# Optimization experiments

Measured on AMD Instinct MI355X. Metric: run time of the kernel, lower is better.

The kernel has to match this reference:

```python
import jax, jax.numpy as jnp
import numpy as np

EPS = 1e-12  # torch F.normalize default eps

def l2norm(x, axis):
    n = jnp.sqrt(jnp.sum(x * x, axis=axis, keepdims=True))
    return x / jnp.maximum(n, EPS)

def conv2d(x, w, b, pad):
    y = jax.lax.conv_general_dilated(x, w, (1, 1), [(pad, pad), (pad, pad)],
                                     dimension_numbers=('NCHW', 'OIHW', 'NCHW'))
    return y + b[None, :, None, None]

def setup_inputs() -> dict:
    key = jax.random.key(0)
    ks = jax.random.split(key, 12)
    N, C, H, W, K = 16, 256, 64, 64, 32
    s = 0.05
    return {
        'feature':   jax.random.normal(ks[0], (N, C, H, W), jnp.float32),
        'conv_up_w': jax.random.normal(ks[1], (K, C, 3, 3), jnp.float32) * s,
        'conv_up_b': jax.random.normal(ks[2], (K,), jnp.float32) * s,
        'centroids': jax.random.uniform(ks[3], (K, C), jnp.float32),
        'upfc_w':    jax.random.normal(ks[4], (C, K * C), jnp.float32) * s,
        'upfc_b':    jax.random.normal(ks[5], (C,), jnp.float32) * s,
        't1_w':      jax.random.normal(ks[6], (C, 2 * C, 1, 1), jnp.float32) * s,
        't1_b':      jax.random.normal(ks[7], (C,), jnp.float32) * s,
        't2_w':      jax.random.normal(ks[8], (C, C, 1, 1), jnp.float32) * s,
        't2_b':      jax.random.normal(ks[9], (C,), jnp.float32) * s,
    }

def reference(feature, conv_up_w, conv_up_b, centroids, upfc_w, upfc_b, t1_w, t1_b, t2_w, t2_b):
    N, C, H, W = feature.shape
    K = centroids.shape[0]
    # --- UP branch ---
    xn = l2norm(feature, axis=1)                       # (N,C,H,W)
    sa = jax.nn.softmax(conv2d(xn, conv_up_w, conv_up_b, 1), axis=1)  # (N,K,H,W)
    sa_flat = sa.reshape(N, K, H * W)                  # (N,K,L)
    x_flat = xn.reshape(N, C, H * W)                   # (N,C,L)
    # sum_l sa[n,k,l] * (x[n,c,l] - centroid[k,c])  ==  two matmuls, no (N,K,C,L) tensor
    up = jnp.einsum('nkl,ncl->nkc', sa_flat, x_flat) \
         - jnp.sum(sa_flat, axis=-1)[:, :, None] * centroids[None]   # (N,K,C)
    up = l2norm(up, axis=2).reshape(N, K * C)
    up = l2norm(up, axis=1)
    up = up @ upfc_w.T + upfc_b                        # (N,C)
    up_map = jnp.broadcast_to(up[:, :, None, None], (N, C, H, W))
    # --- transform ---
    nf = jnp.concatenate([feature, up_map], axis=1)    # (N,2C,H,W)
    h = jax.nn.relu(conv2d(nf, t1_w, t1_b, 0))
    return jax.nn.relu(conv2d(h, t2_w, t2_b, 0))
```

## Files before the change

### kernel.cpp

```cpp
#include <hip/hip_runtime.h>
#include <cstdint>

#define N_ 16
#define C_ 256
#define H_ 64
#define W_ 64
#define L_ 4096
#define K_ 32
#define CL_ (C_*L_)
#define KL_ (K_*L_)
#define KC_ (K_*C_)

typedef __attribute__((ext_vector_type(8))) short short8;
typedef __attribute__((ext_vector_type(4))) float f32x4;

__device__ __forceinline__ unsigned short f2bf(float x) {
    unsigned int u = __float_as_uint(x);
    u += 0x7fffu + ((u >> 16) & 1u);
    return (unsigned short)(u >> 16);
}
__device__ __forceinline__ unsigned int pack2(float a, float b) {
    return (unsigned int)f2bf(a) | ((unsigned int)f2bf(b) << 16);
}

__device__ __forceinline__ void glds16(const void* g, void* l) {
    __builtin_amdgcn_global_load_lds(
        (const __attribute__((address_space(1))) unsigned int*)g,
        (__attribute__((address_space(3))) unsigned int*)l, 16, 0, 0);
}

__global__ __launch_bounds__(256) void k_prep(
    const float* __restrict__ f, float* __restrict__ rinv,
    unsigned short* __restrict__ xnb)
{
    __shared__ float tile[256 * 34];
    __shared__ float ssred[8 * 33];
    __shared__ float rbuf[32];
    int bid = blockIdx.x;
    int n = bid >> 7;
    int l0 = (bid & 127) << 5;
    int tid = threadIdx.x;
    int l = tid & 31, cb = tid >> 5;
    const float* fp = f + (size_t)n * CL_ + l0 + l;
    float ss = 0.f;
#pragma unroll
    for (int i = 0; i < 32; ++i) {
        int c = (cb << 5) + i;
        float v = fp[(size_t)c * L_];
        tile[c * 34 + l] = v;
        ss = fmaf(v, v, ss);
    }
    ssred[cb * 33 + l] = ss;
    __syncthreads();
    if (tid < 32) {
        float s = 0.f;
#pragma unroll
        for (int j = 0; j < 8; ++j) s += ssred[j * 33 + tid];
        float ri = 1.0f / fmaxf(sqrtf(s), 1e-12f);
        rinv[n * L_ + l0 + tid] = ri;
        rbuf[tid] = ri;
    }
    __syncthreads();
    float ri = rbuf[l];
    unsigned short* op = xnb + ((size_t)n * L_ + l0 + l) * C_ + (cb << 5);
#pragma unroll
    for (int g = 0; g < 4; ++g) {
        unsigned int pk[4];
#pragma unroll
        for (int d = 0; d < 4; ++d) {
            int c = (cb << 5) + (g << 3) + (d << 1);
            pk[d] = pack2(tile[c * 34 + l] * ri, tile[(c + 1) * 34 + l] * ri);
        }
        *(uint4*)(op + (g << 3)) = make_uint4(pk[0], pk[1], pk[2], pk[3]);
    }
}

__global__ __launch_bounds__(256) void k_wpack(const float* __restrict__ w, unsigned short* __restrict__ wb) {
    int i = blockIdx.x * 256 + threadIdx.x;
    int j = i & 7;
    int k = (i >> 3) & 31;
    int q = (i >> 8) & 3;
    int ch = (i >> 10) & 7;
    int t = i >> 13;
    int c = (ch << 5) + (q << 3) + j;
    wb[i] = f2bf(w[k * 2304 + c * 9 + t]);
}

__global__ __launch_bounds__(256) void k_wpack2(const float* __restrict__ w, int stride,
                                                unsigned short* __restrict__ wb) {
    int i = blockIdx.x * 256 + threadIdx.x;
    int co = i >> 8, ci = i & 255;
    wb[i] = f2bf(w[(size_t)co * stride + ci]);
}

__global__ __launch_bounds__(128, 2) void k_conv(
    const unsigned short* __restrict__ xnb, const unsigned short* __restrict__ wb,
    const float* __restrict__ bias, const float* __restrict__ zpad,
    float* __restrict__ sa, float* __restrict__ ssum)
{
    __shared__ __align__(16) unsigned short lsB[2][408 * 8];
    __shared__ __align__(16) unsigned short lsW[2][1152 * 8];
    __shared__ float sred[2][32];
    int bid = blockIdx.x;
    int n = bid & 15, y = (bid >> 4) & 63, px_b = bid >> 10;
    int tid = threadIdx.x;
    int wv = tid >> 6, lane = tid & 63;
    int r = lane & 15, quad = lane >> 4;
    int pxw = (wv << 4) + r;
    int xbase = (px_b << 5) - 1;
    const unsigned short* xb = xnb + (size_t)n * CL_;
    const unsigned short* zp = (const unsigned short*)zpad;

    const unsigned short* bsrc[4];
    bool bact[4];
#pragma unroll
    for (int k = 0; k < 4; ++k) {
        int c = (wv << 6) + (k << 7) + lane;
        bool act = c < 408;
        int cc = act ? c : 0;
        int row = cc / 136;
        int rem = cc - row * 136;
        int q = rem / 34;
        int px = rem - q * 34;
        int yy = y + row - 1, xx = xbase + px;
        bool ok = act && ((unsigned)yy < 64u) && ((unsigned)xx < 64u);
        bsrc[k] = ok ? (xb + (((size_t)(yy << 6) + xx) << 8) + (q << 3)) : zp;
        bact[k] = act;
    }

    f32x4 acc0 = (f32x4){0.f, 0.f, 0.f, 0.f};
    f32x4 acc1 = (f32x4){0.f, 0.f, 0.f, 0.f};

    {
#pragma unroll
        for (int k = 0; k < 4; ++k)
            if (bact[k]) glds16(bsrc[k], lsB[0] + (((wv << 6) + (k << 7)) << 3));
#pragma unroll
        for (int k = 0; k < 9; ++k) {
            int idx = wv * 9 + k;
            int t = idx >> 1, h = idx & 1;
            glds16(wb + (t << 13) + (h << 9) + (lane << 3), lsW[0] + (idx << 9));
        }
    }

    for (int i = 0; i < 8; ++i) {
        asm volatile("s_waitcnt vmcnt(0)" ::: "memory");
        __syncthreads();
        if (i < 7) {
            int c1 = (i + 1) << 5;
            unsigned short* dB = lsB[(i + 1) & 1];
            unsigned short* dW = lsW[(i + 1) & 1];
#pragma unroll
            for (int k = 0; k < 4; ++k)
                if (bact[k]) glds16(bsrc[k] + c1, dB + (((wv << 6) + (k << 7)) << 3));
#pragma unroll
            for (int k = 0; k < 9; ++k) {
                int idx = wv * 9 + k;
                int t = idx >> 1, h = idx & 1;
                glds16(wb + (t << 13) + (h << 9) + ((i + 1) << 10) + (lane << 3),
                       dW + (idx << 9));
            }
        }
        const unsigned short* bufB = lsB[i & 1];
        const unsigned short* bufW = lsW[i & 1];
#pragma unroll
        for (int dy = 0; dy < 3; ++dy) {
#pragma unroll
            for (int dx = 0; dx < 3; ++dx) {
                int t = dy * 3 + dx;
                short8 B  = *(const short8*)(bufB + ((((dy << 2) + quad) * 34 + (pxw + dx)) << 3));
                short8 A0 = *(const short8*)(bufW + (((t << 7) + (quad << 5) + r) << 3));
                short8 A1 = *(const short8*)(bufW + (((t << 7) + (quad << 5) + 16 + r) << 3));
                acc0 = __builtin_amdgcn_mfma_f32_16x16x32_bf16(A0, B, acc0, 0, 0, 0);
                acc1 = __builtin_amdgcn_mfma_f32_16x16x32_bf16(A1, B, acc1, 0, 0, 0);
            }
        }
    }
    float4 b0 = *(const float4*)(bias + (quad << 2));
    float4 b1 = *(const float4*)(bias + 16 + (quad << 2));
    float v[8];
    v[0] = acc0[0] + b0.x; v[1] = acc0[1] + b0.y; v[2] = acc0[2] + b0.z; v[3] = acc0[3] + b0.w;
    v[4] = acc1[0] + b1.x; v[5] = acc1[1] + b1.y; v[6] = acc1[2] + b1.z; v[7] = acc1[3] + b1.w;
    float mx = v[0];
#pragma unroll
    for (int j = 1; j < 8; ++j) mx = fmaxf(mx, v[j]);
    mx = fmaxf(mx, __shfl_xor(mx, 16));
    mx = fmaxf(mx, __shfl_xor(mx, 32));
    float s = 0.f;
#pragma unroll
    for (int j = 0; j < 8; ++j) { v[j] = __expf(v[j] - mx); s += v[j]; }
    s += __shfl_xor(s, 16);
    s += __shfl_xor(s, 32);
    float rs = 1.0f / s;
    float sv8[8];
#pragma unroll
    for (int j = 0; j < 8; ++j) sv8[j] = v[j] * rs;
    int l = (y << 6) + (px_b << 5) + pxw;
    float* sp = sa + (size_t)n * KL_ + l;
#pragma unroll
    for (int j = 0; j < 4; ++j) {
        sp[(size_t)((quad << 2) + j) * L_] = sv8[j];
        sp[(size_t)(16 + (quad << 2) + j) * L_] = sv8[4 + j];
    }
#pragma unroll
    for (int j = 0; j < 8; ++j) {
        float a = sv8[j];
        a += __shfl_xor(a, 1); a += __shfl_xor(a, 2);
        a += __shfl_xor(a, 4); a += __shfl_xor(a, 8);
        sv8[j] = a;
    }
    if (r == 0) {
#pragma unroll
        for (int j = 0; j < 4; ++j) {
            sred[wv][(quad << 2) + j] = sv8[j];
            sred[wv][16 + (quad << 2) + j] = sv8[4 + j];
        }
    }
    __syncthreads();
    if (tid < 32) {
        float t = sred[0][tid] + sred[1][tid];
        atomicAdd(ssum + n * K_ + tid, t);
    }
}

__global__ __launch_bounds__(256) void k_einsum(
    const float* __restrict__ f, const float* __restrict__ rinv,
    const float* __restrict__ sa, float* __restrict__ up)
{
    __shared__ float xn_s[C_ * 33];
    __shared__ float sa_s[K_ * 32];
    int bid = blockIdx.x;
    int n = bid >> 5;
    int l0 = (bid & 31) << 7;
    int tid = threadIdx.x;
    int kq = tid >> 5, cq = tid & 31;
    float acc[4][8];
#pragma unroll
    for (int i = 0; i < 4; ++i)
#pragma unroll
        for (int j = 0; j < 8; ++j) acc[i][j] = 0.f;

    for (int ch = 0; ch < 4; ++ch) {
        int lc = l0 + (ch << 5);
        __syncthreads();
        {
            int crow = tid >> 3, lq = (tid & 7) << 2;
#pragma unroll
            for (int p = 0; p < 8; ++p) {
                int c = (p << 5) + crow;
                float4 f4 = *(const float4*)(f + (size_t)n * CL_ + (size_t)c * L_ + lc + lq);
                float4 r4 = *(const float4*)(rinv + n * L_ + lc + lq);
                float* d = xn_s + c * 33 + lq;
                d[0] = f4.x * r4.x; d[1] = f4.y * r4.y; d[2] = f4.z * r4.z; d[3] = f4.w * r4.w;
            }
        }
        {
            int k = tid >> 3, lq = (tid & 7) << 2;
            float4 a4 = *(const float4*)(sa + (size_t)n * KL_ + (size_t)k * L_ + lc + lq);
            *(float4*)(sa_s + (k << 5) + lq) = a4;
        }
        __syncthreads();
#pragma unroll 4
        for (int l = 0; l < 32; ++l) {
            float sv[4], xv[8];
#pragma unroll
            for (int i = 0; i < 4; ++i) sv[i] = sa_s[((kq << 2) + i) * 32 + l];
#pragma unroll
            for (int j = 0; j < 8; ++j) xv[j] = xn_s[(cq + (j << 5)) * 33 + l];
#pragma unroll
            for (int i = 0; i < 4; ++i)
#pragma unroll
                for (int j = 0; j < 8; ++j) acc[i][j] = fmaf(sv[i], xv[j], acc[i][j]);
        }
    }
    float* upp = up + (size_t)n * KC_;
#pragma unroll
    for (int i = 0; i < 4; ++i)
#pragma unroll
        for (int j = 0; j < 8; ++j)
            atomicAdd(upp + ((kq << 2) + i) * C_ + cq + (j << 5), acc[i][j]);
}

__global__ __launch_bounds__(256) void k_rowfix(
    const float* __restrict__ up, const float* __restrict__ ssum,
    const float* __restrict__ cent, float* __restrict__ upn, float* __restrict__ rowss)
{
    __shared__ float red[256];
    int bid = blockIdx.x;
    int k = bid & 31;
    float sv = ssum[bid];
    float v = up[(size_t)bid * C_ + threadIdx.x] - sv * cent[k * C_ + threadIdx.x];
    red[threadIdx.x] = v * v; __syncthreads();
    for (int st = 128; st > 0; st >>= 1) {
        if (threadIdx.x < st) red[threadIdx.x] += red[threadIdx.x + st];
        __syncthreads();
    }
    float ss = red[0];
    float ri = 1.0f / fmaxf(sqrtf(ss), 1e-12f);
    upn[(size_t)bid * C_ + threadIdx.x] = v * ri;
    if (threadIdx.x == 0) rowss[bid] = ss * ri * ri;
}

__global__ __launch_bounds__(256) void k_fc(
    const float* __restrict__ upn, const float* __restrict__ rowss,
    const float* __restrict__ w, const float* __restrict__ b,
    float* __restrict__ upvec)
{
    __shared__ float rnb[16];
    __shared__ float red[16][5];
    int c = blockIdx.x;
    int tid = threadIdx.x;
    int wv = tid >> 6, lane = tid & 63;
    if (tid < 16) {
        float ts = 0.f;
#pragma unroll
        for (int k = 0; k < K_; ++k) ts += rowss[(tid << 5) + k];
        rnb[tid] = 1.0f / fmaxf(sqrtf(ts), 1e-12f);
    }
    float acc[16];
#pragma unroll
    for (int n = 0; n < 16; ++n) acc[n] = 0.f;
    const float* wr = w + (size_t)c * KC_;
#pragma unroll
    for (int g = 0; g < 8; ++g) {
        int kc = (g << 10) + (tid << 2);
        float4 w4 = *(const float4*)(wr + kc);
#pragma unroll
        for (int n = 0; n < 16; ++n) {
            float4 u4 = *(const float4*)(upn + n * KC_ + kc);
            acc[n] += w4.x * u4.x + w4.y * u4.y + w4.z * u4.z + w4.w * u4.w;
        }
    }
#pragma unroll
    for (int n = 0; n < 16; ++n) {
        float a = acc[n];
#pragma unroll
        for (int s = 1; s < 64; s <<= 1) a += __shfl_xor(a, s);
        if (lane == 0) red[n][wv] = a;
    }
    __syncthreads();
    if (tid < 16) {
        float v = red[tid][0] + red[tid][1] + red[tid][2] + red[tid][3];
        upvec[tid * C_ + c] = v * rnb[tid] + b[c];
    }
}

__global__ __launch_bounds__(256) void k_t1up(
    const float* __restrict__ upvec, const float* __restrict__ t1w,
    const float* __restrict__ t1b, float* __restrict__ t1up)
{
    __shared__ float wld[256];
    int co = blockIdx.x;
    int tid = threadIdx.x;
    wld[tid] = t1w[(size_t)co * 512 + 256 + tid];
    __syncthreads();
    int n = tid >> 4, s = tid & 15;
    float a = 0.f;
#pragma unroll
    for (int i = 0; i < 16; ++i)
        a += wld[s + (i << 4)] * upvec[n * C_ + s + (i << 4)];
#pragma unroll
    for (int st = 1; st < 16; st <<= 1) a += __shfl_xor(a, st);
    if (s == 0) t1up[n * C_ + co] = a + t1b[co];
}

__global__ __launch_bounds__(256) void k_gemm1(
    const float* __restrict__ f, const unsigned short* __restrict__ wb,
    const float* __restrict__ t1up, unsigned short* __restrict__ hb)
{
    __shared__ __align__(16) unsigned int lsB[2][128 * 20];
    int bid = blockIdx.x;
    int co_b = bid & 1, px_b = (bid >> 1) & 31, n = bid >> 6;
    int l0 = px_b << 7;
    int tid = threadIdx.x;
    int wv = tid >> 6, lane = tid & 63;
    int r = lane & 15, quad = lane >> 4;
    int pxl = (wv >> 1) << 6;
    int co0 = (co_b << 7) + ((wv & 1) << 6);
    const float* fb_ = f + (size_t)n * CL_ + l0;
    int c2 = tid & 15, pxg = tid >> 4;

    unsigned int pk[2][4];
#pragma unroll
    for (int k2 = 0; k2 < 2; ++k2) {
        const float* s0 = fb_ + (size_t)(c2 << 1) * L_ + ((pxg + (k2 << 4)) << 2);
        float4 a = *(const float4*)s0;
        float4 b = *(const float4*)(s0 + L_);
        pk[k2][0] = pack2(a.x, b.x); pk[k2][1] = pack2(a.y, b.y);
        pk[k2][2] = pack2(a.z, b.z); pk[k2][3] = pack2(a.w, b.w);
    }
    f32x4 acc[4][4];
#pragma unroll
    for (int i = 0; i < 4; ++i)
#pragma unroll
        for (int j = 0; j < 4; ++j) acc[i][j] = (f32x4){0.f, 0.f, 0.f, 0.f};

    for (int i = 0; i < 8; ++i) {
        int c0 = i << 5;
        unsigned int* buf = lsB[i & 1];
#pragma unroll
        for (int k2 = 0; k2 < 2; ++k2) {
            int base = (pxg + (k2 << 4)) * 80 + c2;
            buf[base]      = pk[k2][0];
            buf[base + 20] = pk[k2][1];
            buf[base + 40] = pk[k2][2];
            buf[base + 60] = pk[k2][3];
        }
        __syncthreads();
        if (i < 7) {
#pragma unroll
            for (int k2 = 0; k2 < 2; ++k2) {
                const float* s0 = fb_ + (size_t)(c0 + 32 + (c2 << 1)) * L_ + ((pxg + (k2 << 4)) << 2);
                float4 a = *(const float4*)s0;
                float4 b = *(const float4*)(s0 + L_);
                pk[k2][0] = pack2(a.x, b.x); pk[k2][1] = pack2(a.y, b.y);
                pk[k2][2] = pack2(a.z, b.z); pk[k2][3] = pack2(a.w, b.w);
            }
        }
        short8 A[4], B[4];
#pragma unroll
        for (int t = 0; t < 4; ++t)
            A[t] = *(const short8*)(wb + (size_t)(co0 + (t << 4) + r) * C_ + c0 + (quad << 3));
#pragma unroll
        for (int t = 0; t < 4; ++t)
            B[t] = *(const short8*)((const unsigned short*)buf + (pxl + (t << 4) + r) * 40 + (quad << 3));
#pragma unroll
        for (int pxt = 0; pxt < 4; ++pxt)
#pragma unroll
            for (int cot = 0; cot < 4; ++cot)
                acc[pxt][cot] = __builtin_amdgcn_mfma_f32_16x16x32_bf16(A[cot], B[pxt], acc[pxt][cot], 0, 0, 0);
    }
#pragma unroll
    for (int pxt = 0; pxt < 4; ++pxt) {
        int px = l0 + pxl + (pxt << 4) + r;
        unsigned short* orow = hb + ((size_t)n * L_ + px) * C_;
#pragma unroll
        for (int cot = 0; cot < 4; ++cot) {
            int cb = co0 + (cot << 4) + (quad << 2);
            float4 bb = *(const float4*)(t1up + n * C_ + cb);
            unsigned int p0 = pack2(fmaxf(acc[pxt][cot][0] + bb.x, 0.f),
                                    fmaxf(acc[pxt][cot][1] + bb.y, 0.f));
            unsigned int p1 = pack2(fmaxf(acc[pxt][cot][2] + bb.z, 0.f),
                                    fmaxf(acc[pxt][cot][3] + bb.w, 0.f));
            *(uint2*)(orow + cb) = make_uint2(p0, p1);
        }
    }
}

__global__ __launch_bounds__(256) void k_gemm2(
    const unsigned short* __restrict__ hb, const unsigned short* __restrict__ wb,
    const float* __restrict__ t2b, float* __restrict__ out)
{
    __shared__ __align__(16) unsigned short lsB[2][128 * 40];
    int bid = blockIdx.x;
    int co_b = bid & 1, px_b = (bid >> 1) & 31, n = bid >> 6;
    int l0 = px_b << 7;
    int tid = threadIdx.x;
    int wv = tid >> 6, lane = tid & 63;
    int r = lane & 15, quad = lane >> 4;
    int pxl = (wv >> 1) << 6;
    int co0 = (co_b << 7) + ((wv & 1) << 6);
    const unsigned short* hrow = hb + ((size_t)n * L_ + l0) * C_;
    int q = tid & 3, pxs = tid >> 2;

    uint4 pre[2];
#pragma unroll
    for (int k2 = 0; k2 < 2; ++k2)
        pre[k2] = *(const uint4*)(hrow + (size_t)(pxs + (k2 << 6)) * C_ + (q << 3));

    f32x4 acc[4][4];
#pragma unroll
    for (int i = 0; i < 4; ++i)
#pragma unroll
        for (int j = 0; j < 4; ++j) acc[i][j] = (f32x4){0.f, 0.f, 0.f, 0.f};

    for (int i = 0; i < 8; ++i) {
        int c0 = i << 5;
        unsigned short* buf = lsB[i & 1];
#pragma unroll
        for (int k2 = 0; k2 < 2; ++k2)
            *(uint4*)(buf + (pxs + (k2 << 6)) * 40 + (q << 3)) = pre[k2];
        __syncthreads();
        if (i < 7) {
#pragma unroll
            for (int k2 = 0; k2 < 2; ++k2)
                pre[k2] = *(const uint4*)(hrow + (size_t)(pxs + (k2 << 6)) * C_ + c0 + 32 + (q << 3));
        }
        short8 A[4], B[4];
#pragma unroll
        for (int t = 0; t < 4; ++t)
            A[t] = *(const short8*)(wb + (size_t)(co0 + (t << 4) + r) * C_ + c0 + (quad << 3));
#pragma unroll
        for (int t = 0; t < 4; ++t)
            B[t] = *(const short8*)(buf + (pxl + (t << 4) + r) * 40 + (quad << 3));
#pragma unroll
        for (int pxt = 0; pxt < 4; ++pxt)
#pragma unroll
            for (int cot = 0; cot < 4; ++cot)
                acc[pxt][cot] = __builtin_amdgcn_mfma_f32_16x16x32_bf16(A[cot], B[pxt], acc[pxt][cot], 0, 0, 0);
    }
#pragma unroll
    for (int pxt = 0; pxt < 4; ++pxt) {
        int px = l0 + pxl + (pxt << 4) + r;
#pragma unroll
        for (int cot = 0; cot < 4; ++cot) {
            int cb = co0 + (cot << 4) + (quad << 2);
            float4 bb = *(const float4*)(t2b + cb);
            out[((size_t)n * C_ + cb + 0) * L_ + px] = fmaxf(acc[pxt][cot][0] + bb.x, 0.f);
            out[((size_t)n * C_ + cb + 1) * L_ + px] = fmaxf(acc[pxt][cot][1] + bb.y, 0.f);
            out[((size_t)n * C_ + cb + 2) * L_ + px] = fmaxf(acc[pxt][cot][2] + bb.z, 0.f);
            out[((size_t)n * C_ + cb + 3) * L_ + px] = fmaxf(acc[pxt][cot][3] + bb.w, 0.f);
        }
    }
}

extern "C" void kernel_launch(void* const* d_in, const int* in_sizes, int n_in,
                              void* d_out, int out_size, void* d_ws, size_t ws_size,
                              hipStream_t stream)
{
    const float* feature = (const float*)d_in[0];
    const float* conv_w  = (const float*)d_in[1];
    const float* conv_b  = (const float*)d_in[2];
    const float* cent    = (const float*)d_in[3];
    const float* upfc_w  = (const float*)d_in[4];
    const float* upfc_b  = (const float*)d_in[5];
    const float* t1w     = (const float*)d_in[6];
    const float* t1b     = (const float*)d_in[7];
    const float* t2w     = (const float*)d_in[8];
    const float* t2b     = (const float*)d_in[9];

    float* ws = (float*)d_ws;
    unsigned short* xnb = (unsigned short*)ws;
    unsigned short* hb  = xnb;
    float* rest  = ws + 8388608;
    float* rinv  = rest;
    float* sa    = rinv + 65536;
    float* up    = sa + 2097152;
    float* ssum  = up + 131072;
    float* zpad  = ssum + 512;
    float* upn   = zpad + 512;
    float* rowss = upn + 131072;
    float* upvec = rowss + 512;
    float* t1up  = upvec + 4096;
    unsigned short* wbconv = (unsigned short*)upn;
    unsigned short* t1wb = (unsigned short*)sa;
    unsigned short* t2wb = t1wb + 65536;
    float* out = (float*)d_out;

    hipMemsetAsync(up, 0, (131072 + 512 + 512) * sizeof(float), stream);
    k_prep     <<<2048, 256, 0, stream>>>(feature, rinv, xnb);
    k_wpack    <<<288,  256, 0, stream>>>(conv_w, wbconv);
    k_conv     <<<2048, 128, 0, stream>>>(xnb, wbconv, conv_b, zpad, sa, ssum);
    k_einsum   <<<512,  256, 0, stream>>>(feature, rinv, sa, up);
    k_rowfix   <<<512,  256, 0, stream>>>(up, ssum, cent, upn, rowss);
    k_wpack2   <<<256,  256, 0, stream>>>(t1w, 512, t1wb);
    k_wpack2   <<<256,  256, 0, stream>>>(t2w, 256, t2wb);
    k_fc       <<<256,  256, 0, stream>>>(upn, rowss, upfc_w, upfc_b, upvec);
    k_t1up     <<<256,  256, 0, stream>>>(upvec, t1w, t1b, t1up);
    k_gemm1    <<<1024, 256, 0, stream>>>(feature, t1wb, t1up, hb);
    k_gemm2    <<<1024, 256, 0, stream>>>(hb, t2wb, t2b, out);
}
```

Measured before the change: 310.7 us.

## Stage 1x1-conv GEMM weights and activations into LDS via direct global-to-LDS loads

The t1/t2 weight packing now uses a chunked layout (ci-chunk, quad, co, 8) so each wave can copy contiguous 16-byte rows straight into shared memory with glds16. k_gemm1 double-buffers the weight tiles in LDS instead of reading A fragments from global memory each iteration, and it delays the bf16 packing of feature values until the store. k_gemm2 stages both the hb activations and the weights through async global-to-LDS copies, with an explicit vmcnt wait before each barrier. The aim is to cut repeated global weight reads and register-staged copies, at the cost of more LDS use and full-drain waits that may limit overlap.

```diff
diff --git a/kernel.cpp b/kernel.cpp
--- a/kernel.cpp
+++ b/kernel.cpp
@@ -86,11 +86,12 @@
     wb[i] = f2bf(w[k * 2304 + c * 9 + t]);
 }
 
-__global__ __launch_bounds__(256) void k_wpack2(const float* __restrict__ w, int stride,
-                                                unsigned short* __restrict__ wb) {
+__global__ __launch_bounds__(256) void k_wpackp(const float* __restrict__ w, int stride,
+                                                unsigned short* __restrict__ wb2) {
     int i = blockIdx.x * 256 + threadIdx.x;
-    int co = i >> 8, ci = i & 255;
-    wb[i] = f2bf(w[(size_t)co * stride + ci]);
+    int j = i & 7, co = (i >> 3) & 255, q = (i >> 11) & 3, ch = i >> 13;
+    int ci = (ch << 5) + (q << 3) + j;
+    wb2[i] = f2bf(w[(size_t)co * stride + ci]);
 }
 
 __global__ __launch_bounds__(128, 2) void k_conv(
@@ -365,10 +366,11 @@
 }
 
 __global__ __launch_bounds__(256) void k_gemm1(
-    const float* __restrict__ f, const unsigned short* __restrict__ wb,
+    const float* __restrict__ f, const unsigned short* __restrict__ wb2,
     const float* __restrict__ t1up, unsigned short* __restrict__ hb)
 {
     __shared__ __align__(16) unsigned int lsB[2][128 * 20];
+    __shared__ __align__(16) unsigned short lsW[2][512 * 8];
     int bid = blockIdx.x;
     int co_b = bid & 1, px_b = (bid >> 1) & 31, n = bid >> 6;
     int l0 = px_b << 7;
@@ -376,19 +378,23 @@
     int wv = tid >> 6, lane = tid & 63;
     int r = lane & 15, quad = lane >> 4;
     int pxl = (wv >> 1) << 6;
-    int co0 = (co_b << 7) + ((wv & 1) << 6);
+    int co0l = (wv & 1) << 6;
+    int co0 = (co_b << 7) + co0l;
     const float* fb_ = f + (size_t)n * CL_ + l0;
     int c2 = tid & 15, pxg = tid >> 4;
 
-    unsigned int pk[2][4];
+    float4 ra[2], rb[2];
 #pragma unroll
     for (int k2 = 0; k2 < 2; ++k2) {
         const float* s0 = fb_ + (size_t)(c2 << 1) * L_ + ((pxg + (k2 << 4)) << 2);
-        float4 a = *(const float4*)s0;
-        float4 b = *(const float4*)(s0 + L_);
-        pk[k2][0] = pack2(a.x, b.x); pk[k2][1] = pack2(a.y, b.y);
-        pk[k2][2] = pack2(a.z, b.z); pk[k2][3] = pack2(a.w, b.w);
-    }
+        ra[k2] = *(const float4*)s0;
+        rb[k2] = *(const float4*)(s0 + L_);
+    }
+#pragma unroll
+    for (int k = 0; k < 2; ++k)
+        glds16(wb2 + (((wv << 8) + (co_b << 7) + (k << 6) + lane) << 3),
+               lsW[0] + (((wv << 7) + (k << 6)) << 3));
+
     f32x4 acc[4][4];
 #pragma unroll
     for (int i = 0; i < 4; ++i)
@@ -396,8 +402,13 @@
         for (int j = 0; j < 4; ++j) acc[i][j] = (f32x4){0.f, 0.f, 0.f, 0.f};
 
     for (int i = 0; i < 8; ++i) {
-        int c0 = i << 5;
         unsigned int* buf = lsB[i & 1];
+        unsigned int pk[2][4];
+#pragma unroll
+        for (int k2 = 0; k2 < 2; ++k2) {
+            pk[k2][0] = pack2(ra[k2].x, rb[k2].x); pk[k2][1] = pack2(ra[k2].y, rb[k2].y);
+            pk[k2][2] = pack2(ra[k2].z, rb[k2].z); pk[k2][3] = pack2(ra[k2].w, rb[k2].w);
+        }
 #pragma unroll
         for (int k2 = 0; k2 < 2; ++k2) {
             int base = (pxg + (k2 << 4)) * 80 + c2;
@@ -406,21 +417,25 @@
             buf[base + 40] = pk[k2][2];
             buf[base + 60] = pk[k2][3];
         }
+        asm volatile("s_waitcnt vmcnt(0)" ::: "memory");
         __syncthreads();
         if (i < 7) {
 #pragma unroll
             for (int k2 = 0; k2 < 2; ++k2) {
-                const float* s0 = fb_ + (size_t)(c0 + 32 + (c2 << 1)) * L_ + ((pxg + (k2 << 4)) << 2);
-                float4 a = *(const float4*)s0;
-                float4 b = *(const float4*)(s0 + L_);
-                pk[k2][0] = pack2(a.x, b.x); pk[k2][1] = pack2(a.y, b.y);
-                pk[k2][2] = pack2(a.z, b.z); pk[k2][3] = pack2(a.w, b.w);
+                const float* s0 = fb_ + (size_t)(((i + 1) << 5) + (c2 << 1)) * L_ + ((pxg + (k2 << 4)) << 2);
+                ra[k2] = *(const float4*)s0;
+                rb[k2] = *(const float4*)(s0 + L_);
             }
-        }
+#pragma unroll
+            for (int k = 0; k < 2; ++k)
+                glds16(wb2 + ((((((i + 1) << 2) + wv) << 8) + (co_b << 7) + (k << 6) + lane) << 3),
+                       lsW[(i + 1) & 1] + (((wv << 7) + (k << 6)) << 3));
+        }
+        const unsigned short* bufW = lsW[i & 1];
         short8 A[4], B[4];
 #pragma unroll
         for (int t = 0; t < 4; ++t)
-            A[t] = *(const short8*)(wb + (size_t)(co0 + (t << 4) + r) * C_ + c0 + (quad << 3));
+            A[t] = *(const short8*)(bufW + (((quad << 7) + co0l + (t << 4) + r) << 3));
 #pragma unroll
         for (int t = 0; t < 4; ++t)
             B[t] = *(const short8*)((const unsigned short*)buf + (pxl + (t << 4) + r) * 40 + (quad << 3));
@@ -448,10 +463,11 @@
 }
 
 __global__ __launch_bounds__(256) void k_gemm2(
-    const unsigned short* __restrict__ hb, const unsigned short* __restrict__ wb,
+    const unsigned short* __restrict__ hb, const unsigned short* __restrict__ wb2,
     const float* __restrict__ t2b, float* __restrict__ out)
 {
-    __shared__ __align__(16) unsigned short lsB[2][128 * 40];
+    __shared__ __align__(16) unsigned short lsB[2][512 * 8];
+    __shared__ __align__(16) unsigned short lsW[2][512 * 8];
     int bid = blockIdx.x;
     int co_b = bid & 1, px_b = (bid >> 1) & 31, n = bid >> 6;
     int l0 = px_b << 7;
@@ -459,14 +475,17 @@
     int wv = tid >> 6, lane = tid & 63;
     int r = lane & 15, quad = lane >> 4;
     int pxl = (wv >> 1) << 6;
-    int co0 = (co_b << 7) + ((wv & 1) << 6);
+    int co0l = (wv & 1) << 6;
+    int co0 = (co_b << 7) + co0l;
     const unsigned short* hrow = hb + ((size_t)n * L_ + l0) * C_;
-    int q = tid & 3, pxs = tid >> 2;
-
-    uint4 pre[2];
-#pragma unroll
-    for (int k2 = 0; k2 < 2; ++k2)
-        pre[k2] = *(const uint4*)(hrow + (size_t)(pxs + (k2 << 6)) * C_ + (q << 3));
+
+#pragma unroll
+    for (int k = 0; k < 2; ++k) {
+        glds16(hrow + (size_t)((k << 6) + lane) * C_ + (wv << 3),
+               lsB[0] + (((wv << 7) + (k << 6)) << 3));
+        glds16(wb2 + (((wv << 8) + (co_b << 7) + (k << 6) + lane) << 3),
+               lsW[0] + (((wv << 7) + (k << 6)) << 3));
+    }
 
     f32x4 acc[4][4];
 #pragma unroll
@@ -475,24 +494,26 @@
         for (int j = 0; j < 4; ++j) acc[i][j] = (f32x4){0.f, 0.f, 0.f, 0.f};
 
     for (int i = 0; i < 8; ++i) {
-        int c0 = i << 5;
-        unsigned short* buf = lsB[i & 1];
-#pragma unroll
-        for (int k2 = 0; k2 < 2; ++k2)
-            *(uint4*)(buf + (pxs + (k2 << 6)) * 40 + (q << 3)) = pre[k2];
+        asm volatile("s_waitcnt vmcnt(0)" ::: "memory");
         __syncthreads();
         if (i < 7) {
 #pragma unroll
-            for (int k2 = 0; k2 < 2; ++k2)
-                pre[k2] = *(const uint4*)(hrow + (size_t)(pxs + (k2 << 6)) * C_ + c0 + 32 + (q << 3));
-        }
+            for (int k = 0; k < 2; ++k) {
+                glds16(hrow + (size_t)((k << 6) + lane) * C_ + ((i + 1) << 5) + (wv << 3),
+                       lsB[(i + 1) & 1] + (((wv << 7) + (k << 6)) << 3));
+                glds16(wb2 + ((((((i + 1) << 2) + wv) << 8) + (co_b << 7) + (k << 6) + lane) << 3),
+                       lsW[(i + 1) & 1] + (((wv << 7) + (k << 6)) << 3));
+            }
+        }
+        const unsigned short* bufB = lsB[i & 1];
+        const unsigned short* bufW = lsW[i & 1];
         short8 A[4], B[4];
 #pragma unroll
         for (int t = 0; t < 4; ++t)
-            A[t] = *(const short8*)(wb + (size_t)(co0 + (t << 4) + r) * C_ + c0 + (quad << 3));
+            A[t] = *(const short8*)(bufW + (((quad << 7) + co0l + (t << 4) + r) << 3));
 #pragma unroll
         for (int t = 0; t < 4; ++t)
-            B[t] = *(const short8*)(buf + (pxl + (t << 4) + r) * 40 + (quad << 3));
+            B[t] = *(const short8*)(bufB + (((quad << 7) + pxl + (t << 4) + r) << 3));
 #pragma unroll
         for (int pxt = 0; pxt < 4; ++pxt)
 #pragma unroll
@@ -553,8 +574,8 @@
     k_conv     <<<2048, 128, 0, stream>>>(xnb, wbconv, conv_b, zpad, sa, ssum);
     k_einsum   <<<512,  256, 0, stream>>>(feature, rinv, sa, up);
     k_rowfix   <<<512,  256, 0, stream>>>(up, ssum, cent, upn, rowss);
-    k_wpack2   <<<256,  256, 0, stream>>>(t1w, 512, t1wb);
-    k_wpack2   <<<256,  256, 0, stream>>>(t2w, 256, t2wb);
+    k_wpackp   <<<256,  256, 0, stream>>>(t1w, 512, t1wb);
+    k_wpackp   <<<256,  256, 0, stream>>>(t2w, 256, t2wb);
     k_fc       <<<256,  256, 0, stream>>>(upn, rowss, upfc_w, upfc_b, upvec);
     k_t1up     <<<256,  256, 0, stream>>>(upvec, t1w, t1b, t1up);
     k_gemm1    <<<1024, 256, 0, stream>>>(feature, t1wb, t1up, hb);
```

After: 299.8 us. -3.5%, faster.
